# Kernel tuning notes

Measured on AMD Instinct MI355X. Metric: run time of the kernel, lower is better.

## Reference

```python
import jax, jax.numpy as jnp
import numpy as np

N, E, IN, H, D = 50000, 800000, 128, 4, 32
NEG_SLOPE = 0.2


def setup_inputs() -> dict:
    key = jax.random.key(0)
    ks = jax.random.split(key, 7)
    feat = jax.random.normal(ks[0], (N, IN), dtype=jnp.float32)
    src = jax.random.randint(ks[1], (E,), 0, N)
    dst = jax.random.randint(ks[2], (E,), 0, N)
    fc_w = jax.random.normal(ks[3], (H * D, IN), dtype=jnp.float32) * 0.05
    attn_l = jax.random.normal(ks[4], (H, D), dtype=jnp.float32) * 0.05
    attn_r = jax.random.normal(ks[5], (H, D), dtype=jnp.float32) * 0.05
    res_w = jax.random.normal(ks[6], (H * D, IN), dtype=jnp.float32) * 0.05
    return {"feat": feat, "src": src, "dst": dst, "fc_w": fc_w,
            "attn_l": attn_l, "attn_r": attn_r, "res_w": res_w}


def reference(feat, src, dst, fc_w, attn_l, attn_r, res_w):
    # Shared linear projection: [N, H, D]
    h = (feat @ fc_w.T).reshape(N, H, D)
    # Per-node attention logits: el (source side), er (destination side), [N, H]
    el = jnp.einsum("nhd,hd->nh", h, attn_l)
    er = jnp.einsum("nhd,hd->nh", h, attn_r)
    # Per-edge score and exp (original uses plain exp, no max-subtraction)
    e = jax.nn.leaky_relu(el[src] + er[dst], negative_slope=NEG_SLOPE)  # [E, H]
    coeff = jnp.exp(e)
    # Softmax denominator per destination node
    denom = jax.ops.segment_sum(coeff, dst, num_segments=N)  # [N, H]
    alpha = coeff / denom[dst]  # [E, H]
    # Weighted aggregation of source features into destinations: [N, H, D]
    msg = alpha[:, :, None] * h[src]  # [E, H, D]
    rst = jax.ops.segment_sum(msg, dst, num_segments=N)
    # Residual projection (always applied in this module)
    resval = (feat @ res_w.T).reshape(N, H, D)
    return rst + resval
```

## Files before the change

### kernel.cpp

```cpp
#include <hip/hip_runtime.h>
#include <hip/hip_bf16.h>

#define NN 50000
#define EE 800000
#define HH 4
#define HDIM 128
#define CAP 64
#define CSTR 16

#define GEMM_BLOCKS ((NN + 63) / 64)
#define CHUNKS      (EE / 4)
#define GRP_BLOCKS  ((CHUNKS + 255) / 256)
#define ZERO_BLOCKS ((NN * CSTR) / 256)
#define W16_BLOCKS  16

typedef __attribute__((ext_vector_type(8))) short bf16x8;
typedef __attribute__((ext_vector_type(4))) float f32x4;
typedef __attribute__((ext_vector_type(4))) int  intv4;

__device__ inline unsigned short f2bf(float f) {
    unsigned u = __float_as_uint(f);
    u = u + 0x7FFFu + ((u >> 16) & 1u);
    return (unsigned short)(u >> 16);
}
__device__ inline float bfl(unsigned u) { return __uint_as_float(u << 16); }
__device__ inline float bfh(unsigned u) { return __uint_as_float(u & 0xFFFF0000u); }

__global__ void zero_kernel(int* __restrict__ cnt) {
    int idx = blockIdx.x * 256 + threadIdx.x;
    if (idx < NN * CSTR) cnt[idx] = 0;
}

__global__ void scatter_kernel(const int* __restrict__ src,
                               const int* __restrict__ dst,
                               int* __restrict__ cnt,
                               int* __restrict__ perm_src,
                               const float* __restrict__ fc_w,
                               const float* __restrict__ res_w,
                               unsigned short* __restrict__ w16) {
    if (blockIdx.x >= 8 * GRP_BLOCKS) {
        int idx = (blockIdx.x - 8 * GRP_BLOCKS) * 256 + threadIdx.x;
        int base = idx * 8;
        if (base < 256 * 128) {
            const float* sw = (base < 128 * 128) ? &fc_w[base] : &res_w[base - 128 * 128];
            float4 v0 = *(const float4*)&sw[0];
            float4 v1 = *(const float4*)&sw[4];
            unsigned short tmp[8] = { f2bf(v0.x), f2bf(v0.y), f2bf(v0.z), f2bf(v0.w),
                                      f2bf(v1.x), f2bf(v1.y), f2bf(v1.z), f2bf(v1.w) };
            *(uint4*)&w16[base] = *(uint4*)tmp;
        }
        return;
    }
    int g = blockIdx.x & 7;
    int cidx = (blockIdx.x >> 3) * 256 + threadIdx.x;
    int e4 = cidx * 4;
    if (e4 >= EE) return;
    intv4 s4 = __builtin_nontemporal_load((const intv4*)&src[e4]);
    intv4 d4 = __builtin_nontemporal_load((const intv4*)&dst[e4]);
    if ((d4.x & 7) == g) {
        int p = atomicAdd(&cnt[d4.x * CSTR], 1);
        if (p < CAP) perm_src[d4.x * CAP + p] = s4.x;
    }
    if ((d4.y & 7) == g) {
        int p = atomicAdd(&cnt[d4.y * CSTR], 1);
        if (p < CAP) perm_src[d4.y * CAP + p] = s4.y;
    }
    if ((d4.z & 7) == g) {
        int p = atomicAdd(&cnt[d4.z * CSTR], 1);
        if (p < CAP) perm_src[d4.z * CAP + p] = s4.z;
    }
    if ((d4.w & 7) == g) {
        int p = atomicAdd(&cnt[d4.w * CSTR], 1);
        if (p < CAP) perm_src[d4.w * CAP + p] = s4.w;
    }
}

__global__ __launch_bounds__(256) void gemm_elr_kernel(const float* __restrict__ feat,
                                                       const unsigned short* __restrict__ w16,
                                                       const float* __restrict__ al,
                                                       const float* __restrict__ ar,
                                                       unsigned short* __restrict__ h16,
                                                       unsigned short* __restrict__ res16,
                                                       float* __restrict__ el,
                                                       float* __restrict__ er,
                                                       int n) {
    __shared__ unsigned short As[64][136];
    __shared__ unsigned short Hs[64][136];
    int t = threadIdx.x;
    int w = t >> 6;
    int l = t & 63;
    int l15 = l & 15;
    int kg = l >> 4;
    int r0 = blockIdx.x * 64;
    int colbase = w * 64;

    bf16x8 bfrag[4][4];
    #pragma unroll
    for (int ct = 0; ct < 4; ++ct) {
        int col = colbase + ct * 16 + l15;
        #pragma unroll
        for (int ks = 0; ks < 4; ++ks)
            bfrag[ct][ks] = *(const bf16x8*)&w16[(size_t)col * 128 + ks * 32 + kg * 8];
    }

    for (int i = t; i < 64 * 32; i += 256) {
        int r = i >> 5;
        int c4 = (i & 31) << 2;
        float4 v = make_float4(0.f, 0.f, 0.f, 0.f);
        if (r0 + r < n) v = *(const float4*)&feat[(size_t)(r0 + r) * 128 + c4];
        unsigned short tmp[4] = { f2bf(v.x), f2bf(v.y), f2bf(v.z), f2bf(v.w) };
        *(uint2*)&As[r][c4] = *(uint2*)tmp;
    }
    __syncthreads();

    f32x4 acc[4][4];
    #pragma unroll
    for (int rt = 0; rt < 4; ++rt)
        #pragma unroll
        for (int ct = 0; ct < 4; ++ct)
            acc[rt][ct] = (f32x4){0.f, 0.f, 0.f, 0.f};

    #pragma unroll
    for (int ks = 0; ks < 4; ++ks) {
        bf16x8 afrag[4];
        #pragma unroll
        for (int rt = 0; rt < 4; ++rt)
            afrag[rt] = *(const bf16x8*)&As[rt * 16 + l15][ks * 32 + kg * 8];
        #pragma unroll
        for (int rt = 0; rt < 4; ++rt)
            #pragma unroll
            for (int ct = 0; ct < 4; ++ct)
                acc[rt][ct] = __builtin_amdgcn_mfma_f32_16x16x32_bf16(
                    afrag[rt], bfrag[ct][ks], acc[rt][ct], 0, 0, 0);
    }
    __syncthreads();

    int rb = 4 * kg;
    if (w < 2) {
        #pragma unroll
        for (int rt = 0; rt < 4; ++rt)
            #pragma unroll
            for (int ct = 0; ct < 4; ++ct)
                #pragma unroll
                for (int r = 0; r < 4; ++r)
                    Hs[rt * 16 + rb + r][colbase + ct * 16 + l15] = f2bf(acc[rt][ct][r]);
    } else {
        #pragma unroll
        for (int rt = 0; rt < 4; ++rt)
            #pragma unroll
            for (int ct = 0; ct < 4; ++ct)
                #pragma unroll
                for (int r = 0; r < 4; ++r)
                    As[rt * 16 + rb + r][(colbase - 128) + ct * 16 + l15] = f2bf(acc[rt][ct][r]);
    }
    __syncthreads();

    #pragma unroll
    for (int it = 0; it < 4; ++it) {
        int flat = it * 2048 + t * 8;
        int row = flat >> 7;
        int col = flat & 127;
        if (r0 + row < n) {
            *(uint4*)&h16[(size_t)(r0 + row) * 128 + col] = *(const uint4*)&Hs[row][col];
            *(uint4*)&res16[(size_t)(r0 + row) * 128 + col] = *(const uint4*)&As[row][col];
        }
    }

    int node = t >> 2;
    int hh = t & 3;
    if (r0 + node < n) {
        const unsigned short* hp = &Hs[node][hh * 32];
        const float* alp = &al[hh * 32];
        const float* arp = &ar[hh * 32];
        float a = 0.f, b = 0.f;
        #pragma unroll
        for (int c = 0; c < 4; ++c) {
            uint4 hv = *(const uint4*)&hp[c * 8];
            unsigned uu[4] = { hv.x, hv.y, hv.z, hv.w };
            #pragma unroll
            for (int j = 0; j < 4; ++j) {
                float v0 = bfl(uu[j]);
                float v1 = bfh(uu[j]);
                int d = c * 8 + j * 2;
                a = fmaf(v0, alp[d], a);     a = fmaf(v1, alp[d + 1], a);
                b = fmaf(v0, arp[d], b);     b = fmaf(v1, arp[d + 1], b);
            }
        }
        el[(size_t)(r0 + node) * 4 + hh] = a;
        er[(size_t)(r0 + node) * 4 + hh] = b;
    }
}

__global__ __launch_bounds__(256) void gather_agg_kernel(const int* __restrict__ cnt,
                                                         const int* __restrict__ perm_src,
                                                         const float* __restrict__ el,
                                                         const float* __restrict__ er,
                                                         const unsigned short* __restrict__ h16,
                                                         const unsigned short* __restrict__ res16,
                                                         float* __restrict__ out) {
    __shared__ int   Ss[8][CAP];
    __shared__ float Cs[8][CAP][HH];
    int t = threadIdx.x;
    int nl = t >> 5;
    int node = blockIdx.x * 8 + nl;
    int ln = t & 31;
    int d0 = ln << 2;
    int hh = ln >> 3;
    int q  = ln & 7;
    int deg = cnt[node * CSTR];
    if (deg > CAP) deg = CAP;
    int o0 = node * CAP;
    float erh = er[node * 4 + hh];

    float dsum = 0.f;
    for (int j = q; j < deg; j += 8) {
        int s = perm_src[o0 + j];
        if (hh == 0) Ss[nl][j] = s;
        float x = el[s * 4 + hh] + erh;
        x = (x > 0.f) ? x : 0.2f * x;
        float c = __expf(x);
        Cs[nl][j][hh] = c;
        dsum += c;
    }
    dsum += __shfl_xor(dsum, 1, 64);
    dsum += __shfl_xor(dsum, 2, 64);
    dsum += __shfl_xor(dsum, 4, 64);
    float inv = (deg > 0) ? 1.0f / dsum : 0.f;
    __syncthreads();

    float4 acc = make_float4(0.f, 0.f, 0.f, 0.f);
    int j = 0;
    for (; j + 7 < deg; j += 8) {
        uint2 hv[8];
        float cc[8];
        #pragma unroll
        for (int k = 0; k < 8; ++k) {
            int s = Ss[nl][j + k];
            cc[k] = Cs[nl][j + k][hh];
            hv[k] = *(const uint2*)&h16[(size_t)s * 128 + d0];
        }
        #pragma unroll
        for (int k = 0; k < 8; ++k) {
            acc.x = fmaf(cc[k], bfl(hv[k].x), acc.x);
            acc.y = fmaf(cc[k], bfh(hv[k].x), acc.y);
            acc.z = fmaf(cc[k], bfl(hv[k].y), acc.z);
            acc.w = fmaf(cc[k], bfh(hv[k].y), acc.w);
        }
    }
    for (; j + 3 < deg; j += 4) {
        uint2 hv[4];
        float cc[4];
        #pragma unroll
        for (int k = 0; k < 4; ++k) {
            int s = Ss[nl][j + k];
            cc[k] = Cs[nl][j + k][hh];
            hv[k] = *(const uint2*)&h16[(size_t)s * 128 + d0];
        }
        #pragma unroll
        for (int k = 0; k < 4; ++k) {
            acc.x = fmaf(cc[k], bfl(hv[k].x), acc.x);
            acc.y = fmaf(cc[k], bfh(hv[k].x), acc.y);
            acc.z = fmaf(cc[k], bfl(hv[k].y), acc.z);
            acc.w = fmaf(cc[k], bfh(hv[k].y), acc.w);
        }
    }
    for (; j < deg; ++j) {
        int s0 = Ss[nl][j];
        float c0 = Cs[nl][j][hh];
        uint2 h0 = *(const uint2*)&h16[(size_t)s0 * 128 + d0];
        acc.x = fmaf(c0, bfl(h0.x), acc.x); acc.y = fmaf(c0, bfh(h0.x), acc.y);
        acc.z = fmaf(c0, bfl(h0.y), acc.z); acc.w = fmaf(c0, bfh(h0.y), acc.w);
    }
    size_t oidx = (size_t)node * 128 + d0;
    uint2 rv = *(const uint2*)&res16[oidx];
    float4 res;
    res.x = fmaf(acc.x, inv, bfl(rv.x));
    res.y = fmaf(acc.y, inv, bfh(rv.x));
    res.z = fmaf(acc.z, inv, bfl(rv.y));
    res.w = fmaf(acc.w, inv, bfh(rv.y));
    *(float4*)&out[oidx] = res;
}

extern "C" void kernel_launch(void* const* d_in, const int* in_sizes, int n_in,
                              void* d_out, int out_size, void* d_ws, size_t ws_size,
                              hipStream_t stream) {
    const float* feat   = (const float*)d_in[0];
    const int*   src    = (const int*)d_in[1];
    const int*   dst    = (const int*)d_in[2];
    const float* fc_w   = (const float*)d_in[3];
    const float* attn_l = (const float*)d_in[4];
    const float* attn_r = (const float*)d_in[5];
    const float* res_w  = (const float*)d_in[6];
    float* out = (float*)d_out;

    unsigned short* h16   = (unsigned short*)d_ws;
    unsigned short* res16 = h16 + (size_t)NN * HDIM;
    float* el  = (float*)(res16 + (size_t)NN * HDIM);
    float* er  = el + (size_t)NN * HH;
    unsigned short* w16 = (unsigned short*)(er + (size_t)NN * HH);
    int*   perm_src = (int*)(w16 + 256 * 128);
    int*   cnt      = perm_src + (size_t)NN * CAP;

    zero_kernel<<<ZERO_BLOCKS, 256, 0, stream>>>(cnt);

    scatter_kernel<<<8 * GRP_BLOCKS + W16_BLOCKS, 256, 0, stream>>>(
        src, dst, cnt, perm_src, fc_w, res_w, w16);

    gemm_elr_kernel<<<GEMM_BLOCKS, 256, 0, stream>>>(feat, w16, attn_l, attn_r,
                                                     h16, res16, el, er, NN);

    gather_agg_kernel<<<NN / 8, 256, 0, stream>>>(cnt, perm_src, el, er, h16, res16, out);
}
```

Measured before the change: 112.6 us.

## Fuse edge scatter with GEMM in one launch and merge zero/weight-convert kernels

Merges the counter zeroing and weight bf16 conversion into a single prep kernel. The edge scatter, which buckets edges by destination with atomics, now runs in the same launch as the projection GEMM. Blocks are split by index so three of every four super-blocks run a grid-stride scatter loop and the fourth runs GEMM tiles. The aim is to overlap the atomic-bound scatter with the compute-bound GEMM and to cut launch overhead, at the cost of a hand-tuned block split that may balance poorly.

```diff
diff --git a/kernel.cpp b/kernel.cpp
--- a/kernel.cpp
+++ b/kernel.cpp
@@ -10,9 +10,12 @@
 
 #define GEMM_BLOCKS ((NN + 63) / 64)
 #define CHUNKS      (EE / 4)
-#define GRP_BLOCKS  ((CHUNKS + 255) / 256)
 #define ZERO_BLOCKS ((NN * CSTR) / 256)
 #define W16_BLOCKS  16
+
+#define SB_TOT   392
+#define SCAT_SB  294
+#define FUSED_BLOCKS (SB_TOT * 8)
 
 typedef __attribute__((ext_vector_type(8))) short bf16x8;
 typedef __attribute__((ext_vector_type(4))) float f32x4;
@@ -26,20 +29,17 @@
 __device__ inline float bfl(unsigned u) { return __uint_as_float(u << 16); }
 __device__ inline float bfh(unsigned u) { return __uint_as_float(u & 0xFFFF0000u); }
 
-__global__ void zero_kernel(int* __restrict__ cnt) {
-    int idx = blockIdx.x * 256 + threadIdx.x;
-    if (idx < NN * CSTR) cnt[idx] = 0;
-}
-
-__global__ void scatter_kernel(const int* __restrict__ src,
-                               const int* __restrict__ dst,
-                               int* __restrict__ cnt,
-                               int* __restrict__ perm_src,
-                               const float* __restrict__ fc_w,
-                               const float* __restrict__ res_w,
-                               unsigned short* __restrict__ w16) {
-    if (blockIdx.x >= 8 * GRP_BLOCKS) {
-        int idx = (blockIdx.x - 8 * GRP_BLOCKS) * 256 + threadIdx.x;
+__global__ void prep_kernel(int* __restrict__ cnt,
+                            const float* __restrict__ fc_w,
+                            const float* __restrict__ res_w,
+                            unsigned short* __restrict__ w16) {
+    int bx = blockIdx.x;
+    int t = threadIdx.x;
+    if (bx < ZERO_BLOCKS) {
+        int idx = bx * 256 + t;
+        if (idx < NN * CSTR) cnt[idx] = 0;
+    } else {
+        int idx = (bx - ZERO_BLOCKS) * 256 + t;
         int base = idx * 8;
         if (base < 256 * 128) {
             const float* sw = (base < 128 * 128) ? &fc_w[base] : &res_w[base - 128 * 128];
@@ -49,49 +49,62 @@
                                       f2bf(v1.x), f2bf(v1.y), f2bf(v1.z), f2bf(v1.w) };
             *(uint4*)&w16[base] = *(uint4*)tmp;
         }
-        return;
-    }
-    int g = blockIdx.x & 7;
-    int cidx = (blockIdx.x >> 3) * 256 + threadIdx.x;
-    int e4 = cidx * 4;
-    if (e4 >= EE) return;
-    intv4 s4 = __builtin_nontemporal_load((const intv4*)&src[e4]);
-    intv4 d4 = __builtin_nontemporal_load((const intv4*)&dst[e4]);
-    if ((d4.x & 7) == g) {
-        int p = atomicAdd(&cnt[d4.x * CSTR], 1);
-        if (p < CAP) perm_src[d4.x * CAP + p] = s4.x;
-    }
-    if ((d4.y & 7) == g) {
-        int p = atomicAdd(&cnt[d4.y * CSTR], 1);
-        if (p < CAP) perm_src[d4.y * CAP + p] = s4.y;
-    }
-    if ((d4.z & 7) == g) {
-        int p = atomicAdd(&cnt[d4.z * CSTR], 1);
-        if (p < CAP) perm_src[d4.z * CAP + p] = s4.z;
-    }
-    if ((d4.w & 7) == g) {
-        int p = atomicAdd(&cnt[d4.w * CSTR], 1);
-        if (p < CAP) perm_src[d4.w * CAP + p] = s4.w;
-    }
-}
-
-__global__ __launch_bounds__(256) void gemm_elr_kernel(const float* __restrict__ feat,
-                                                       const unsigned short* __restrict__ w16,
-                                                       const float* __restrict__ al,
-                                                       const float* __restrict__ ar,
-                                                       unsigned short* __restrict__ h16,
-                                                       unsigned short* __restrict__ res16,
-                                                       float* __restrict__ el,
-                                                       float* __restrict__ er,
-                                                       int n) {
+    }
+}
+
+__global__ __launch_bounds__(256) void fused_kernel(const float* __restrict__ feat,
+                                                    const unsigned short* __restrict__ w16,
+                                                    const float* __restrict__ al,
+                                                    const float* __restrict__ ar,
+                                                    unsigned short* __restrict__ h16,
+                                                    unsigned short* __restrict__ res16,
+                                                    float* __restrict__ el,
+                                                    float* __restrict__ er,
+                                                    const int* __restrict__ src,
+                                                    const int* __restrict__ dst,
+                                                    int* __restrict__ cnt,
+                                                    int* __restrict__ perm_src,
+                                                    int n) {
     __shared__ unsigned short As[64][136];
     __shared__ unsigned short Hs[64][136];
+    int sb = blockIdx.x >> 3;
+    int lane8 = blockIdx.x & 7;
     int t = threadIdx.x;
+
+    if ((sb & 3) != 3) {
+        int scat_sb = sb - (sb >> 2);
+        int g = lane8;
+        for (int cidx = scat_sb * 256 + t; cidx < CHUNKS; cidx += SCAT_SB * 256) {
+            int e4 = cidx * 4;
+            intv4 s4 = __builtin_nontemporal_load((const intv4*)&src[e4]);
+            intv4 d4 = __builtin_nontemporal_load((const intv4*)&dst[e4]);
+            if ((d4.x & 7) == g) {
+                int p = atomicAdd(&cnt[d4.x * CSTR], 1);
+                if (p < CAP) perm_src[d4.x * CAP + p] = s4.x;
+            }
+            if ((d4.y & 7) == g) {
+                int p = atomicAdd(&cnt[d4.y * CSTR], 1);
+                if (p < CAP) perm_src[d4.y * CAP + p] = s4.y;
+            }
+            if ((d4.z & 7) == g) {
+                int p = atomicAdd(&cnt[d4.z * CSTR], 1);
+                if (p < CAP) perm_src[d4.z * CAP + p] = s4.z;
+            }
+            if ((d4.w & 7) == g) {
+                int p = atomicAdd(&cnt[d4.w * CSTR], 1);
+                if (p < CAP) perm_src[d4.w * CAP + p] = s4.w;
+            }
+        }
+        return;
+    }
+
+    int gemm_id = (sb >> 2) * 8 + lane8;
+    if (gemm_id >= GEMM_BLOCKS) return;
     int w = t >> 6;
     int l = t & 63;
     int l15 = l & 15;
     int kg = l >> 4;
-    int r0 = blockIdx.x * 64;
+    int r0 = gemm_id * 64;
     int colbase = w * 64;
 
     bf16x8 bfrag[4][4];
@@ -301,13 +314,11 @@
     int*   perm_src = (int*)(w16 + 256 * 128);
     int*   cnt      = perm_src + (size_t)NN * CAP;
 
-    zero_kernel<<<ZERO_BLOCKS, 256, 0, stream>>>(cnt);
-
-    scatter_kernel<<<8 * GRP_BLOCKS + W16_BLOCKS, 256, 0, stream>>>(
-        src, dst, cnt, perm_src, fc_w, res_w, w16);
-
-    gemm_elr_kernel<<<GEMM_BLOCKS, 256, 0, stream>>>(feat, w16, attn_l, attn_r,
-                                                     h16, res16, el, er, NN);
+    prep_kernel<<<ZERO_BLOCKS + W16_BLOCKS, 256, 0, stream>>>(cnt, fc_w, res_w, w16);
+
+    fused_kernel<<<FUSED_BLOCKS, 256, 0, stream>>>(feat, w16, attn_l, attn_r,
+                                                   h16, res16, el, er,
+                                                   src, dst, cnt, perm_src, NN);
 
     gather_agg_kernel<<<NN / 8, 256, 0, stream>>>(cnt, perm_src, el, er, h16, res16, out);
 }
```

After: 125.5 us. 1.12x slower.
